# Optimization experiments

Measured on AMD Instinct MI355X. Metric: run time of the kernel, lower is better.

Reference implementation:

```python
import jax, jax.numpy as jnp
import numpy as np
from jax import lax

B, C, H, W = 2, 128, 192, 192
HEADS, WS, SS = 4, 8, 4
HID = 256  # int(C * expansion=2.0)
EPS = 1e-6


def _rpe_index(ws):
    coords = np.stack(np.meshgrid(np.arange(ws), np.arange(ws), indexing='ij')).reshape(2, -1)
    rel = (coords[:, :, None] - coords[:, None, :]).transpose(1, 2, 0)
    rel[:, :, 0] += ws - 1
    rel[:, :, 1] += ws - 1
    rel[:, :, 0] *= 2 * ws - 1
    return rel.sum(-1)  # (ws^2, ws^2) int index into rpe_table

RPE_IDX = _rpe_index(WS)


def _attn_mask(hp, wp, ws, ss):
    # Swin-style shifted-window mask, built once for static (hp, wp).
    img = np.zeros((hp, wp))
    cnt = 0
    for hs in (slice(0, -ws), slice(-ws, -ss), slice(-ss, None)):
        for wsl in (slice(0, -ws), slice(-ws, -ss), slice(-ss, None)):
            img[hs, wsl] = cnt
            cnt += 1
    mw = img.reshape(hp // ws, ws, wp // ws, ws).transpose(0, 2, 1, 3).reshape(-1, ws * ws)
    am = mw[:, None, :] - mw[:, :, None]
    return np.where(am != 0, -np.inf, 0.0).astype(np.float32)

MASK = jnp.asarray(_attn_mask(H, W, WS, SS))  # (nW, T, T)


def rmsnorm(x, s, b):
    # RMSNorm2d: variance over channel dim, computed in fp32.
    var = jnp.mean(jnp.square(x.astype(jnp.float32)), axis=1, keepdims=True)
    rms = jnp.sqrt(var + EPS).astype(x.dtype)
    return s[None, :, None, None] * x / rms + b[None, :, None, None]


def conv1x1(x, w, b):
    return jnp.einsum('oc,bchw->bohw', w, x) + b[None, :, None, None]


def dwconv3x3(x, w, b):
    y = lax.conv_general_dilated(x, w, (1, 1), 'SAME', feature_group_count=w.shape[0],
                                 dimension_numbers=('NCHW', 'OIHW', 'NCHW'))
    return y + b[None, :, None, None]


def gelu(x):
    return jax.nn.gelu(x, approximate=False)  # matches torch nn.GELU default (erf)


def conv_gated_block(x, s, b, w1, b1, wd, bd, w2, b2, beta):
    y = rmsnorm(x, s, b)
    y = conv1x1(y, w1, b1)
    y = dwconv3x3(y, wd, bd)
    u, v = jnp.split(y, 2, axis=1)
    y = conv1x1(u * gelu(v), w2, b2)
    return x + beta * y


def gated_ffn(x, s, b, w1, b1, w2, b2, gamma):
    y = rmsnorm(x, s, b)
    y = conv1x1(y, w1, b1)
    u, v = jnp.split(y, 2, axis=1)
    y = conv1x1(u * gelu(v), w2, b2)
    return x + gamma * y


def window_attention(x, qkv_w, qkv_b, rpe_table, proj_w, proj_b):
    b, c, h, w = x.shape
    hd = c // HEADS
    ws, ws2 = WS, WS * WS
    # H, W chosen divisible by ws, so _pad_to_window is a no-op here.
    x = jnp.roll(x, (-SS, -SS), axis=(2, 3))
    qkv = jnp.einsum('oc,bchw->bhwo', qkv_w, x) + qkv_b  # (B,H,W,3C)
    qkv = qkv.reshape(b, h // ws, ws, w // ws, ws, 3 * c).transpose(0, 1, 3, 2, 4, 5)
    qkv = qkv.reshape(-1, ws2, 3, HEADS, hd).transpose(2, 0, 3, 1, 4)  # (3, B*nW, nh, T, hd)
    q, k, v = qkv[0], qkv[1], qkv[2]
    attn = jnp.einsum('wnqd,wnkd->wnqk', q, k) * (hd ** -0.5)
    rpe = rpe_table[RPE_IDX.reshape(-1)].reshape(ws2, ws2, HEADS).transpose(2, 0, 1)  # (nh,T,T)
    nW = (h // ws) * (w // ws)
    attn = attn.reshape(b, nW, HEADS, ws2, ws2) + rpe[None, None] + MASK[None, :, None]
    attn = jax.nn.softmax(attn, axis=-1).reshape(-1, HEADS, ws2, ws2)
    out = jnp.einsum('wnqk,wnkd->wnqd', attn, v)
    out = out.transpose(0, 2, 1, 3).reshape(-1, ws2, c)
    out = out @ proj_w.T + proj_b  # nn.Linear
    out = out.reshape(b, h // ws, w // ws, ws, ws, c).transpose(0, 1, 3, 2, 4, 5).reshape(b, h, w, c)
    out = jnp.roll(out, (SS, SS), axis=(1, 2))
    return out.transpose(0, 3, 1, 2)


def setup_inputs():
    key = jax.random.key(0)
    ks = jax.random.split(key, 10)
    f = jnp.float32

    def nrm(k, shape, std=0.02):
        return jax.random.normal(k, shape, dtype=f) * std

    return {
        'x': jax.random.normal(ks[0], (B, C, H, W), dtype=f),
        'cg_s': jnp.ones((C,), f), 'cg_b': jnp.zeros((C,), f),
        'pw1_w': nrm(ks[1], (2 * HID, C)), 'pw1_b': jnp.zeros((2 * HID,), f),
        'dw_w': nrm(ks[2], (2 * HID, 1, 3, 3)), 'dw_b': jnp.zeros((2 * HID,), f),
        'pw2_w': nrm(ks[3], (C, HID)), 'pw2_b': jnp.zeros((C,), f),
        'beta': jnp.float32(0.5),
        'at_s': jnp.ones((C,), f), 'at_b': jnp.zeros((C,), f),
        'qkv_w': nrm(ks[4], (3 * C, C)), 'qkv_b': jnp.zeros((3 * C,), f),
        'rpe_table': nrm(ks[5], ((2 * WS - 1) ** 2, HEADS)),
        'proj_w': nrm(ks[6], (C, C)), 'proj_b': jnp.zeros((C,), f),
        'alpha': jnp.float32(0.5),
        'ff_s': jnp.ones((C,), f), 'ff_b': jnp.zeros((C,), f),
        'fc1_w': nrm(ks[7], (2 * HID, C)), 'fc1_b': jnp.zeros((2 * HID,), f),
        'fc2_w': nrm(ks[8], (C, HID)), 'fc2_b': jnp.zeros((C,), f),
        'gamma': jnp.float32(0.5),
    }


def reference(x, cg_s, cg_b, pw1_w, pw1_b, dw_w, dw_b, pw2_w, pw2_b, beta,
              at_s, at_b, qkv_w, qkv_b, rpe_table, proj_w, proj_b, alpha,
              ff_s, ff_b, fc1_w, fc1_b, fc2_w, fc2_b, gamma):
    x = conv_gated_block(x, cg_s, cg_b, pw1_w, pw1_b, dw_w, dw_b, pw2_w, pw2_b, beta)
    x = x + alpha * window_attention(rmsnorm(x, at_s, at_b), qkv_w, qkv_b, rpe_table, proj_w, proj_b)
    x = gated_ffn(x, ff_s, ff_b, fc1_w, fc1_b, fc2_w, fc2_b, gamma)
    return x
```

## Files before the change

### kernel.cpp

```cpp
#include <hip/hip_runtime.h>
#include <hip/hip_bf16.h>
#include <math.h>

#define HW   36864
#define BHW  73728

typedef float f32x4 __attribute__((ext_vector_type(4)));
typedef short short8 __attribute__((ext_vector_type(8)));
typedef short s16x4 __attribute__((ext_vector_type(4)));

__device__ __forceinline__ unsigned f2bf(float f) {
    unsigned u = __float_as_uint(f);
    return (u + 0x7fffu + ((u >> 16) & 1u)) >> 16;
}
__device__ __forceinline__ float bf2f(unsigned short s) {
    return __uint_as_float(((unsigned)s) << 16);
}
__device__ __forceinline__ float gelu_fast(float x) {
    float y = 1.5957691216057308f * fmaf(0.044715f * x * x, x, x);
    return x / (1.0f + __expf(-y));
}

__global__ __launch_bounds__(256)
void wconv_kernel(const float* __restrict__ w1, const float* __restrict__ w2,
                  const float* __restrict__ wq, const float* __restrict__ wp,
                  const float* __restrict__ wf1, const float* __restrict__ wf2,
                  const float* __restrict__ dww, const float* __restrict__ fb1,
                  ushort* __restrict__ o1, ushort* __restrict__ o2, ushort* __restrict__ oq,
                  ushort* __restrict__ op, ushort* __restrict__ of1, ushort* __restrict__ of2,
                  float* __restrict__ dwt, float* __restrict__ bg)
{
    int i = blockIdx.x * 256 + threadIdx.x;
    if      (i <  65536) o1 [i         ] = (ushort)f2bf(w1 [i         ]);
    else if (i <  98304) o2 [i -  65536] = (ushort)f2bf(w2 [i -  65536]);
    else if (i < 147456) oq [i -  98304] = (ushort)f2bf(wq [i -  98304]);
    else if (i < 163840) op [i - 147456] = (ushort)f2bf(wp [i - 147456]);
    else if (i < 229376) {
        int j = i - 163840;
        int col = j >> 7, k = j & 127;
        of1[j] = (ushort)f2bf(wf1[((size_t)((col & 1) * 256 + (col >> 1))) * 128 + k]);
    }
    else if (i < 262144) of2[i - 229376] = (ushort)f2bf(wf2[i - 229376]);
    else if (i < 266752) {
        int j = i - 262144;
        int tap = j >> 9, c = j & 511;
        dwt[j] = dww[c * 9 + tap];
    }
    else if (i < 267264) {
        int j = i - 266752;
        bg[j] = fb1[(j & 1) * 256 + (j >> 1)];
    }
}

__global__ __launch_bounds__(256)
void rmsnorm_t_kernel(const float* __restrict__ src, const float* __restrict__ s,
                      const float* __restrict__ bi, __hip_bfloat16* __restrict__ dst)
{
    __shared__ float sPar[4][64];
    __shared__ float sInv[64];
    int t = threadIdx.x, lane = t & 63, wv = t >> 6;
    int P = blockIdx.x * 64 + lane;
    int b = P / HW, pp = P - b * HW;
    const float* xb = src + (size_t)b * 128 * HW + pp;
    float v[32];
    float ss = 0.f;
#pragma unroll
    for (int i = 0; i < 32; ++i) {
        float x = xb[(size_t)(wv * 32 + i) * HW];
        v[i] = x;
        ss = fmaf(x, x, ss);
    }
    sPar[wv][lane] = ss;
    __syncthreads();
    if (t < 64) {
        float tot = sPar[0][t] + sPar[1][t] + sPar[2][t] + sPar[3][t];
        sInv[t] = 1.0f / sqrtf(tot * 0.0078125f + 1e-6f);
    }
    __syncthreads();
    float inv = sInv[lane];
    unsigned* drow = (unsigned*)(dst + (size_t)P * 128) + wv * 16;
#pragma unroll
    for (int i = 0; i < 32; i += 2) {
        int c = wv * 32 + i;
        float v0 = fmaf(s[c]     * v[i],     inv, bi[c]);
        float v1 = fmaf(s[c + 1] * v[i + 1], inv, bi[c + 1]);
        drow[i >> 1] = f2bf(v0) | (f2bf(v1) << 16);
    }
}

template<int K, int MODE>
__global__ __launch_bounds__(256, 3)
void gemm_kernel(const __hip_bfloat16* __restrict__ Abf, const __hip_bfloat16* __restrict__ Wbf,
                 const float* __restrict__ bias, int N,
                 __hip_bfloat16* __restrict__ outb)
{
    constexpr int STEPS = K / 32;
    __shared__ __align__(16) short smem[(64 + 128) * K];
    short* sA = smem;
    short* sB = smem + 64 * K;

    const short* A = (const short*)Abf;
    const short* W = (const short*)Wbf;

    int t = threadIdx.x;
    int lane = t & 63, wv = t >> 6;
    int m0 = blockIdx.x * 64;
    int n0 = blockIdx.y * 128;
    int q = lane >> 4, r16 = lane & 15;

    f32x4 acc[4][2];
#pragma unroll
    for (int nt = 0; nt < 2; ++nt) {
        float bv = bias[n0 + wv * 32 + nt * 16 + r16];
#pragma unroll
        for (int mt = 0; mt < 4; ++mt) acc[mt][nt] = (f32x4){bv, bv, bv, bv};
    }

    {
        int lr = lane >> 2, lk = lane & 3;
#pragma unroll
        for (int st = 0; st < STEPS; ++st) {
            int rowA = wv * 16 + lr;
            int kcA = lk ^ ((rowA >> 1) & 3);
            const short* ga = A + (size_t)(m0 + rowA) * K + st * 32 + kcA * 8;
            __builtin_amdgcn_global_load_lds((const __attribute__((address_space(1))) void*)ga,
                                             (__attribute__((address_space(3))) void*)(sA + st * 2048 + wv * 512), 16, 0, 0);
#pragma unroll
            for (int i = 0; i < 2; ++i) {
                int rb = wv * 32 + i * 16;
                int rowB = rb + lr;
                int kcB = lk ^ ((rowB >> 1) & 3);
                const short* gb = W + (size_t)(n0 + rowB) * K + st * 32 + kcB * 8;
                __builtin_amdgcn_global_load_lds((const __attribute__((address_space(1))) void*)gb,
                                                 (__attribute__((address_space(3))) void*)(sB + st * 4096 + rb * 32), 16, 0, 0);
            }
        }
    }
    __syncthreads();

#pragma unroll
    for (int st = 0; st < STEPS; ++st) {
        short8 af[4], bf[2];
#pragma unroll
        for (int mt = 0; mt < 4; ++mt) {
            int r = mt * 16 + r16;
            af[mt] = *(const short8*)(sA + st * 2048 + (r * 4 + (q ^ ((r >> 1) & 3))) * 8);
        }
#pragma unroll
        for (int nt = 0; nt < 2; ++nt) {
            int r = wv * 32 + nt * 16 + r16;
            bf[nt] = *(const short8*)(sB + st * 4096 + (r * 4 + (q ^ ((r >> 1) & 3))) * 8);
        }
#pragma unroll
        for (int mt = 0; mt < 4; ++mt)
#pragma unroll
            for (int nt = 0; nt < 2; ++nt)
                acc[mt][nt] = __builtin_amdgcn_mfma_f32_16x16x32_bf16(af[mt], bf[nt], acc[mt][nt], 0, 0, 0);
    }

    if constexpr (MODE == 0) {
        ushort* ob = (ushort*)outb;
#pragma unroll
        for (int mt = 0; mt < 4; ++mt) {
            int row0 = m0 + mt * 16 + q * 4;
#pragma unroll
            for (int nt = 0; nt < 2; ++nt) {
                int col = n0 + wv * 32 + nt * 16 + r16;
#pragma unroll
                for (int rg = 0; rg < 4; ++rg)
                    ob[(size_t)(row0 + rg) * N + col] = (ushort)f2bf(acc[mt][nt][rg]);
            }
        }
    } else {
        ushort* ob = (ushort*)outb;
        int parity = r16 & 1;
#pragma unroll
        for (int mt = 0; mt < 4; ++mt) {
            int row0 = m0 + mt * 16 + q * 4;
#pragma unroll
            for (int nt = 0; nt < 2; ++nt) {
                int ch = (n0 + wv * 32 + nt * 16 + r16) >> 1;
#pragma unroll
                for (int rg = 0; rg < 4; ++rg) {
                    float val = acc[mt][nt][rg];
                    float part = __shfl_xor(val, 1);
                    float uu = parity ? part : val;
                    float vv = parity ? val : part;
                    float g = uu * gelu_fast(vv);
                    if (!parity)
                        ob[(size_t)(row0 + rg) * 256 + ch] = (ushort)f2bf(g);
                }
            }
        }
    }
}

template<int K, bool RMS>
__global__ __launch_bounds__(256, 3)
void gemm_n128_kernel(const __hip_bfloat16* __restrict__ Abf, const __hip_bfloat16* __restrict__ Wbf,
                      const float* __restrict__ bias,
                      const float* __restrict__ rsrc, float* __restrict__ rdst,
                      const float* __restrict__ scale,
                      const float* __restrict__ rms_s, const float* __restrict__ rms_b,
                      __hip_bfloat16* __restrict__ xn)
{
    constexpr int NH = K / 128;
    __shared__ __align__(16) char smem[49152];
    short* sA = (short*)smem;
    short* sB = sA + 8192;
    float* sEp = (float*)smem;
    float* sPar = (float*)(smem + 34816);
    float* sInv = (float*)(smem + 39168);

    const short* A = (const short*)Abf;
    const short* W = (const short*)Wbf;

    int t = threadIdx.x;
    int lane = t & 63, wv = t >> 6;
    int m0 = blockIdx.x * 64;
    int q = lane >> 4, r16 = lane & 15;

    f32x4 acc[4][2];
#pragma unroll
    for (int nt = 0; nt < 2; ++nt) {
        float bv = bias[wv * 32 + nt * 16 + r16];
#pragma unroll
        for (int mt = 0; mt < 4; ++mt) acc[mt][nt] = (f32x4){bv, bv, bv, bv};
    }

#pragma unroll
    for (int h = 0; h < NH; ++h) {
        if (h) __syncthreads();
        {
            int lr = lane >> 2, lk = lane & 3;
#pragma unroll
            for (int st = 0; st < 4; ++st) {
                int kk = h * 128 + st * 32;
                int rowA = wv * 16 + lr;
                int kcA = lk ^ ((rowA >> 1) & 3);
                const short* ga = A + (size_t)(m0 + rowA) * K + kk + kcA * 8;
                __builtin_amdgcn_global_load_lds((const __attribute__((address_space(1))) void*)ga,
                                                 (__attribute__((address_space(3))) void*)(sA + st * 2048 + wv * 512), 16, 0, 0);
#pragma unroll
                for (int i = 0; i < 2; ++i) {
                    int rb = wv * 32 + i * 16;
                    int rowB = rb + lr;
                    int kcB = lk ^ ((rowB >> 1) & 3);
                    const short* gb = W + (size_t)rowB * K + kk + kcB * 8;
                    __builtin_amdgcn_global_load_lds((const __attribute__((address_space(1))) void*)gb,
                                                     (__attribute__((address_space(3))) void*)(sB + st * 4096 + rb * 32), 16, 0, 0);
                }
            }
        }
        __syncthreads();

#pragma unroll
        for (int st = 0; st < 4; ++st) {
            short8 af[4], bf[2];
#pragma unroll
            for (int mt = 0; mt < 4; ++mt) {
                int r = mt * 16 + r16;
                af[mt] = *(const short8*)(sA + st * 2048 + (r * 4 + (q ^ ((r >> 1) & 3))) * 8);
            }
#pragma unroll
            for (int nt = 0; nt < 2; ++nt) {
                int r = wv * 32 + nt * 16 + r16;
                bf[nt] = *(const short8*)(sB + st * 4096 + (r * 4 + (q ^ ((r >> 1) & 3))) * 8);
            }
#pragma unroll
            for (int mt = 0; mt < 4; ++mt)
#pragma unroll
                for (int nt = 0; nt < 2; ++nt)
                    acc[mt][nt] = __builtin_amdgcn_mfma_f32_16x16x32_bf16(af[mt], bf[nt], acc[mt][nt], 0, 0, 0);
        }
    }
    __syncthreads();

#pragma unroll
    for (int mt = 0; mt < 4; ++mt)
#pragma unroll
        for (int nt = 0; nt < 2; ++nt) {
            int c = wv * 32 + nt * 16 + r16;
            int px = mt * 16 + q * 4;
#pragma unroll
            for (int rg = 0; rg < 4; ++rg)
                sEp[c * 68 + px + rg] = acc[mt][nt][rg];
        }
    __syncthreads();

    int c16 = t >> 4, l16 = t & 15;
    int p0 = m0 + l16 * 4;
    int b = p0 / HW, pp = p0 - b * HW;
    float sc = scale[0];
    f32x4 ov[8];
    f32x4 ps = (f32x4){0.f, 0.f, 0.f, 0.f};
#pragma unroll
    for (int i = 0; i < 8; ++i) {
        int c = c16 + i * 16;
        f32x4 v = *(const f32x4*)&sEp[c * 68 + l16 * 4];
        size_t gi = (size_t)(b * 128 + c) * HW + pp;
        f32x4 r = *(const f32x4*)&rsrc[gi];
        f32x4 o = r + sc * v;
        *(f32x4*)&rdst[gi] = o;
        if constexpr (RMS) {
            ov[i] = o;
#pragma unroll
            for (int rg = 0; rg < 4; ++rg) ps[rg] = fmaf(o[rg], o[rg], ps[rg]);
        }
    }
    if constexpr (RMS) {
#pragma unroll
        for (int rg = 0; rg < 4; ++rg) sPar[(l16 * 4 + rg) * 17 + c16] = ps[rg];
        __syncthreads();
        if (t < 64) {
            float ssum = 0.f;
#pragma unroll
            for (int j = 0; j < 16; ++j) ssum += sPar[t * 17 + j];
            sInv[t] = 1.0f / sqrtf(ssum * 0.0078125f + 1e-6f);
        }
        __syncthreads();
        float iv[4];
#pragma unroll
        for (int rg = 0; rg < 4; ++rg) iv[rg] = sInv[l16 * 4 + rg];
        ushort* sXn = (ushort*)smem;
#pragma unroll
        for (int i = 0; i < 8; ++i) {
            int c = c16 + i * 16;
            float scs = rms_s[c], bcs = rms_b[c];
#pragma unroll
            for (int rg = 0; rg < 4; ++rg)
                sXn[(l16 * 4 + rg) * 132 + c] = (ushort)f2bf(fmaf(scs * ov[i][rg], iv[rg], bcs));
        }
        __syncthreads();
        {
            int px = t >> 2, qd = t & 3;
            const ushort* src = sXn + px * 132 + qd * 32;
            ushort* dst = (ushort*)xn + (size_t)(m0 + px) * 128 + qd * 32;
#pragma unroll
            for (int g = 0; g < 4; ++g)
                *(short8*)(dst + g * 8) = *(const short8*)(src + g * 8);
        }
    }
}

template<bool EDGE>
__device__ __forceinline__ void dw_body(const ushort* __restrict__ t1u,
                                        int b, int h0, int w, int cu,
                                        const f32x4* __restrict__ wu, const f32x4* __restrict__ wv,
                                        f32x4* __restrict__ au, f32x4* __restrict__ av)
{
#pragma unroll
    for (int r = 0; r < 6; ++r) {
        int hh = h0 - 1 + r;
        bool okr = EDGE ? ((unsigned)hh < 192u) : true;
        int hhc = (EDGE && !okr) ? 0 : hh;
#pragma unroll
        for (int dxi = 0; dxi < 3; ++dxi) {
            int w2 = w + dxi - 1;
            bool ok = EDGE ? (okr && ((unsigned)w2 < 192u)) : true;
            int w2c = EDGE ? ((w2 < 0) ? 0 : ((w2 > 191) ? 191 : w2)) : w2;
            const ushort* p = t1u + (size_t)(b * HW + hhc * 192 + w2c) * 512 + cu;
            s16x4 u4 = *(const s16x4*)p;
            s16x4 v4 = *(const s16x4*)(p + 256);
            f32x4 uf, vf;
#pragma unroll
            for (int e = 0; e < 4; ++e) {
                float uu = bf2f((ushort)u4[e]);
                float vv = bf2f((ushort)v4[e]);
                uf[e] = (EDGE && !ok) ? 0.f : uu;
                vf[e] = (EDGE && !ok) ? 0.f : vv;
            }
#pragma unroll
            for (int py = 0; py < 4; ++py) {
                int dy = r - 1 - py;
                if (dy < -1 || dy > 1) continue;
                int tap = (dy + 1) * 3 + dxi;
#pragma unroll
                for (int e = 0; e < 4; ++e) {
                    au[py][e] = fmaf(wu[tap][e], uf[e], au[py][e]);
                    av[py][e] = fmaf(wv[tap][e], vf[e], av[py][e]);
                }
            }
        }
    }
}

__global__ __launch_bounds__(256, 3)
void dwgate_kernel(const __hip_bfloat16* __restrict__ t1, const float* __restrict__ dwt,
                   const float* __restrict__ dwb, __hip_bfloat16* __restrict__ tg)
{
    int t = threadIdx.x;
    int tc = t & 63;
    int tp = t >> 6;
    int bx = blockIdx.x;
    int b = bx / 2304; int tt = bx % 2304;
    int th = tt / 48, tw = tt % 48;
    int h0 = th * 4, w = tw * 4 + tp;
    int cu = tc * 4;
    const ushort* t1u = (const ushort*)t1;

    f32x4 wu[9], wv[9];
#pragma unroll
    for (int tap = 0; tap < 9; ++tap) {
        wu[tap] = *(const f32x4*)(dwt + tap * 512 + cu);
        wv[tap] = *(const f32x4*)(dwt + tap * 512 + 256 + cu);
    }
    f32x4 bu = *(const f32x4*)(dwb + cu);
    f32x4 bv = *(const f32x4*)(dwb + 256 + cu);

    f32x4 au[4], av[4];
#pragma unroll
    for (int py = 0; py < 4; ++py) { au[py] = bu; av[py] = bv; }

    if (th > 0 && th < 47 && tw > 0 && tw < 47)
        dw_body<false>(t1u, b, h0, w, cu, wu, wv, au, av);
    else
        dw_body<true >(t1u, b, h0, w, cu, wu, wv, au, av);

#pragma unroll
    for (int py = 0; py < 4; ++py) {
        s16x4 o4;
#pragma unroll
        for (int e = 0; e < 4; ++e) o4[e] = (short)(ushort)f2bf(au[py][e] * gelu_fast(av[py][e]));
        int gp = b * HW + (h0 + py) * 192 + w;
        *(s16x4*)((ushort*)tg + (size_t)gp * 256 + cu) = o4;
    }
}

__device__ __forceinline__ int wpix(int wh, int ww, int m) {
    int ty = m >> 3, tx = m & 7;
    int hs = wh * 8 + ty + 4; if (hs >= 192) hs -= 192;
    int wsc = ww * 8 + tx + 4; if (wsc >= 192) wsc -= 192;
    return hs * 192 + wsc;
}
__device__ __forceinline__ int wreg(int wh, int ww, int m) {
    int hr = wh * 8 + (m >> 3), wr = ww * 8 + (m & 7);
    return ((hr < 184) ? 0 : (hr < 188) ? 1 : 2) * 3 +
           ((wr < 184) ? 0 : (wr < 188) ? 1 : 2);
}

__global__ __launch_bounds__(256)
void attn_kernel(const __hip_bfloat16* __restrict__ qkv, const float* __restrict__ rpe,
                 __hip_bfloat16* __restrict__ attnout)
{
    __shared__ char smem[54288];
    int t = threadIdx.x;
    int lane = t & 63, head = t >> 6;
    int wh = blockIdx.x / 24, ww = blockIdx.x % 24;
    int b = blockIdx.y;
    int q = lane >> 4, r16 = lane & 15;

    float* rpe_s = (float*)(smem + 50688);
    for (int i = t; i < 900; i += 256) rpe_s[i] = rpe[i];

    char* Pbuf  = smem + head * 12672;
    char* VTbuf = Pbuf + 8448;
    const ushort* qkvu = (const ushort*)qkv;

    short8 aq[4], bk[4];
#pragma unroll
    for (int mt = 0; mt < 4; ++mt) {
        int pix = wpix(wh, ww, mt * 16 + r16);
        const ushort* rowp = qkvu + (size_t)(b * HW + pix) * 384 + head * 32 + q * 8;
        aq[mt] = *(const short8*)rowp;
        bk[mt] = *(const short8*)(rowp + 128);
    }
    {
        int pix = wpix(wh, ww, lane);
        const ushort* vp = qkvu + (size_t)(b * HW + pix) * 384 + 256 + head * 32;
        ushort* vt = (ushort*)VTbuf;
#pragma unroll
        for (int g = 0; g < 4; ++g) {
            short8 v8 = *(const short8*)(vp + g * 8);
#pragma unroll
            for (int e = 0; e < 8; ++e) vt[(g * 8 + e) * 66 + lane] = (ushort)v8[e];
        }
    }
    __syncthreads();

    f32x4 s[4][4];
#pragma unroll
    for (int mt = 0; mt < 4; ++mt)
#pragma unroll
        for (int nt = 0; nt < 4; ++nt) s[mt][nt] = (f32x4){0.f, 0.f, 0.f, 0.f};
#pragma unroll
    for (int mt = 0; mt < 4; ++mt)
#pragma unroll
        for (int nt = 0; nt < 4; ++nt)
            s[mt][nt] = __builtin_amdgcn_mfma_f32_16x16x32_bf16(aq[mt], bk[nt], s[mt][nt], 0, 0, 0);

    bool edge = (wh == 23) || (ww == 23);
    int tyj[4], txj[4], rgj[4];
#pragma unroll
    for (int nt = 0; nt < 4; ++nt) {
        int j = nt * 16 + r16;
        tyj[nt] = j >> 3; txj[nt] = j & 7;
        rgj[nt] = wreg(wh, ww, j);
    }
    float rinv[4][4];
#pragma unroll
    for (int mt = 0; mt < 4; ++mt) {
#pragma unroll
        for (int rg = 0; rg < 4; ++rg) {
            int i = mt * 16 + q * 4 + rg;
            int tyi = i >> 3, txi = i & 7;
            int rgi = edge ? wreg(wh, ww, i) : 0;
            float mx = -INFINITY;
#pragma unroll
            for (int nt = 0; nt < 4; ++nt) {
                float v = s[mt][nt][rg] * 0.17677669529663689f
                        + rpe_s[((tyi - tyj[nt] + 7) * 15 + (txi - txj[nt] + 7)) * 4 + head];
                if (edge && rgi != rgj[nt]) v = -INFINITY;
                s[mt][nt][rg] = v;
                mx = fmaxf(mx, v);
            }
            mx = fmaxf(mx, __shfl_xor(mx, 1));
            mx = fmaxf(mx, __shfl_xor(mx, 2));
            mx = fmaxf(mx, __shfl_xor(mx, 4));
            mx = fmaxf(mx, __shfl_xor(mx, 8));
            float sum = 0.f;
#pragma unroll
            for (int nt = 0; nt < 4; ++nt) {
                float e = __expf(s[mt][nt][rg] - mx);
                s[mt][nt][rg] = e;
                sum += e;
            }
            sum += __shfl_xor(sum, 1);
            sum += __shfl_xor(sum, 2);
            sum += __shfl_xor(sum, 4);
            sum += __shfl_xor(sum, 8);
            rinv[mt][rg] = 1.0f / sum;
        }
    }

    ushort* Pu = (ushort*)Pbuf;
#pragma unroll
    for (int mt = 0; mt < 4; ++mt)
#pragma unroll
        for (int rg = 0; rg < 4; ++rg) {
            int i = mt * 16 + q * 4 + rg;
#pragma unroll
            for (int nt = 0; nt < 4; ++nt)
                Pu[i * 66 + nt * 16 + r16] = (ushort)f2bf(s[mt][nt][rg]);
        }
    __syncthreads();

    f32x4 o[4][2];
#pragma unroll
    for (int mt = 0; mt < 4; ++mt) { o[mt][0] = (f32x4){0,0,0,0}; o[mt][1] = (f32x4){0,0,0,0}; }
    const uint* Pw = (const uint*)Pbuf;
    const uint* Vw = (const uint*)VTbuf;
#pragma unroll
    for (int ks = 0; ks < 2; ++ks) {
        short8 ap[4];
#pragma unroll
        for (int mt = 0; mt < 4; ++mt) {
            int base = (mt * 16 + r16) * 33 + ks * 16 + q * 4;
            uint d0 = Pw[base], d1 = Pw[base + 1], d2 = Pw[base + 2], d3 = Pw[base + 3];
            union { uint u[4]; short8 s8; } cv; cv.u[0] = d0; cv.u[1] = d1; cv.u[2] = d2; cv.u[3] = d3;
            ap[mt] = cv.s8;
        }
        short8 bv[2];
#pragma unroll
        for (int nt = 0; nt < 2; ++nt) {
            int base = (nt * 16 + r16) * 33 + ks * 16 + q * 4;
            uint d0 = Vw[base], d1 = Vw[base + 1], d2 = Vw[base + 2], d3 = Vw[base + 3];
            union { uint u[4]; short8 s8; } cv; cv.u[0] = d0; cv.u[1] = d1; cv.u[2] = d2; cv.u[3] = d3;
            bv[nt] = cv.s8;
        }
#pragma unroll
        for (int mt = 0; mt < 4; ++mt)
#pragma unroll
            for (int nt = 0; nt < 2; ++nt)
                o[mt][nt] = __builtin_amdgcn_mfma_f32_16x16x32_bf16(ap[mt], bv[nt], o[mt][nt], 0, 0, 0);
    }
    __syncthreads();

    float* Of = (float*)Pbuf;
#pragma unroll
    for (int mt = 0; mt < 4; ++mt)
#pragma unroll
        for (int rg = 0; rg < 4; ++rg) {
            int i = mt * 16 + q * 4 + rg;
            float sc = rinv[mt][rg];
            Of[i * 33 + r16]      = o[mt][0][rg] * sc;
            Of[i * 33 + 16 + r16] = o[mt][1][rg] * sc;
        }
    __syncthreads();
    {
        int pix = wpix(wh, ww, lane);
        ushort* ob = (ushort*)attnout + (size_t)(b * HW + pix) * 128 + head * 32;
#pragma unroll
        for (int g = 0; g < 4; ++g) {
            short8 o8;
#pragma unroll
            for (int e = 0; e < 8; ++e) o8[e] = (short)(ushort)f2bf(Of[lane * 33 + g * 8 + e]);
            *(short8*)(ob + g * 8) = o8;
        }
    }
}

extern "C" void kernel_launch(void* const* d_in, const int* in_sizes, int n_in,
                              void* d_out, int out_size, void* d_ws, size_t ws_size,
                              hipStream_t stream)
{
    const float* x     = (const float*)d_in[0];
    const float* cg_s  = (const float*)d_in[1];
    const float* cg_b  = (const float*)d_in[2];
    const float* pw1_w = (const float*)d_in[3];
    const float* pw1_b = (const float*)d_in[4];
    const float* dw_w  = (const float*)d_in[5];
    const float* dw_b  = (const float*)d_in[6];
    const float* pw2_w = (const float*)d_in[7];
    const float* pw2_b = (const float*)d_in[8];
    const float* beta  = (const float*)d_in[9];
    const float* at_s  = (const float*)d_in[10];
    const float* at_b  = (const float*)d_in[11];
    const float* qkv_w = (const float*)d_in[12];
    const float* qkv_b = (const float*)d_in[13];
    const float* rpe   = (const float*)d_in[14];
    const float* proj_w= (const float*)d_in[15];
    const float* proj_b= (const float*)d_in[16];
    const float* alpha = (const float*)d_in[17];
    const float* ff_s  = (const float*)d_in[18];
    const float* ff_b  = (const float*)d_in[19];
    const float* fc1_w = (const float*)d_in[20];
    const float* fc1_b = (const float*)d_in[21];
    const float* fc2_w = (const float*)d_in[22];
    const float* fc2_b = (const float*)d_in[23];
    const float* gamma = (const float*)d_in[24];
    float* out = (float*)d_out;

    char* ws = (char*)d_ws;
    __hip_bfloat16* Xn    = (__hip_bfloat16*)ws;
    __hip_bfloat16* t1    = (__hip_bfloat16*)(ws + 18874368);
    __hip_bfloat16* qkvb  = t1;
    __hip_bfloat16* tg    = (__hip_bfloat16*)(ws + 94371840);
    __hip_bfloat16* attno = tg;
    char* wsw = ws + 132120576;
    ushort* w1b  = (ushort*)(wsw);
    ushort* w2b  = (ushort*)(wsw + 131072);
    ushort* wqb  = (ushort*)(wsw + 196608);
    ushort* wpb  = (ushort*)(wsw + 294912);
    ushort* wf1b = (ushort*)(wsw + 327680);
    ushort* wf2b = (ushort*)(wsw + 458752);
    float*  dwt  = (float*) (wsw + 524288);
    float*  bg1  = (float*) (wsw + 542720);

    wconv_kernel<<<1044, 256, 0, stream>>>(pw1_w, pw2_w, qkv_w, proj_w, fc1_w, fc2_w, dw_w, fc1_b,
                                           w1b, w2b, wqb, wpb, wf1b, wf2b, dwt, bg1);

    rmsnorm_t_kernel<<<1152, 256, 0, stream>>>(x, cg_s, cg_b, Xn);
    gemm_kernel<128, 0><<<dim3(1152, 4), 256, 0, stream>>>(Xn, (__hip_bfloat16*)w1b, pw1_b, 512, t1);
    dwgate_kernel<<<4608, 256, 0, stream>>>(t1, dwt, dw_b, tg);
    gemm_n128_kernel<256, true><<<1152, 256, 0, stream>>>(tg, (__hip_bfloat16*)w2b, pw2_b,
                                                          x, out, beta, at_s, at_b, Xn);

    gemm_kernel<128, 0><<<dim3(1152, 3), 256, 0, stream>>>(Xn, (__hip_bfloat16*)wqb, qkv_b, 384, qkvb);
    attn_kernel<<<dim3(576, 2), 256, 0, stream>>>(qkvb, rpe, attno);
    gemm_n128_kernel<128, true><<<1152, 256, 0, stream>>>(attno, (__hip_bfloat16*)wpb, proj_b,
                                                          out, out, alpha, ff_s, ff_b, Xn);

    gemm_kernel<128, 2><<<dim3(1152, 4), 256, 0, stream>>>(Xn, (__hip_bfloat16*)wf1b, bg1, 512, tg);
    gemm_n128_kernel<256, false><<<1152, 256, 0, stream>>>(tg, (__hip_bfloat16*)wf2b, fc2_b,
                                                           out, out, gamma, nullptr, nullptr, nullptr);
}
```

Before: 360.1 us.

## Load GEMM weight fragments into registers and remap depthwise-gate threads

Result: slower. 446.5 us (+24.0%).

```diff
diff --git a/kernel.cpp b/kernel.cpp
--- a/kernel.cpp
+++ b/kernel.cpp
@@ -6,6 +6,7 @@
 #define BHW  73728
 
 typedef float f32x4 __attribute__((ext_vector_type(4)));
+typedef float f32x2 __attribute__((ext_vector_type(2)));
 typedef short short8 __attribute__((ext_vector_type(8)));
 typedef short s16x4 __attribute__((ext_vector_type(4)));
 
@@ -89,15 +90,13 @@
 }
 
 template<int K, int MODE>
-__global__ __launch_bounds__(256, 3)
+__global__ __launch_bounds__(256, 4)
 void gemm_kernel(const __hip_bfloat16* __restrict__ Abf, const __hip_bfloat16* __restrict__ Wbf,
                  const float* __restrict__ bias, int N,
                  __hip_bfloat16* __restrict__ outb)
 {
     constexpr int STEPS = K / 32;
-    __shared__ __align__(16) short smem[(64 + 128) * K];
-    short* sA = smem;
-    short* sB = smem + 64 * K;
+    __shared__ __align__(16) short sA[64 * K];
 
     const short* A = (const short*)Abf;
     const short* W = (const short*)Wbf;
@@ -108,54 +107,47 @@
     int n0 = blockIdx.y * 128;
     int q = lane >> 4, r16 = lane & 15;
 
-    f32x4 acc[4][2];
-#pragma unroll
-    for (int nt = 0; nt < 2; ++nt) {
-        float bv = bias[n0 + wv * 32 + nt * 16 + r16];
-#pragma unroll
-        for (int mt = 0; mt < 4; ++mt) acc[mt][nt] = (f32x4){bv, bv, bv, bv};
-    }
-
     {
         int lr = lane >> 2, lk = lane & 3;
+        int rowA = wv * 16 + lr;
+        int kcA = lk ^ ((rowA >> 1) & 3);
 #pragma unroll
         for (int st = 0; st < STEPS; ++st) {
-            int rowA = wv * 16 + lr;
-            int kcA = lk ^ ((rowA >> 1) & 3);
             const short* ga = A + (size_t)(m0 + rowA) * K + st * 32 + kcA * 8;
             __builtin_amdgcn_global_load_lds((const __attribute__((address_space(1))) void*)ga,
                                              (__attribute__((address_space(3))) void*)(sA + st * 2048 + wv * 512), 16, 0, 0);
-#pragma unroll
-            for (int i = 0; i < 2; ++i) {
-                int rb = wv * 32 + i * 16;
-                int rowB = rb + lr;
-                int kcB = lk ^ ((rowB >> 1) & 3);
-                const short* gb = W + (size_t)(n0 + rowB) * K + st * 32 + kcB * 8;
-                __builtin_amdgcn_global_load_lds((const __attribute__((address_space(1))) void*)gb,
-                                                 (__attribute__((address_space(3))) void*)(sB + st * 4096 + rb * 32), 16, 0, 0);
-            }
-        }
+        }
+    }
+
+    short8 bfr[STEPS][2];
+#pragma unroll
+    for (int st = 0; st < STEPS; ++st)
+#pragma unroll
+        for (int nt = 0; nt < 2; ++nt)
+            bfr[st][nt] = *(const short8*)(W + (size_t)(n0 + wv * 32 + nt * 16 + r16) * K + st * 32 + q * 8);
+
+    f32x4 acc[4][2];
+#pragma unroll
+    for (int nt = 0; nt < 2; ++nt) {
+        float bv = bias[n0 + wv * 32 + nt * 16 + r16];
+#pragma unroll
+        for (int mt = 0; mt < 4; ++mt) acc[mt][nt] = (f32x4){bv, bv, bv, bv};
     }
     __syncthreads();
 
 #pragma unroll
     for (int st = 0; st < STEPS; ++st) {
-        short8 af[4], bf[2];
+        short8 af[4];
 #pragma unroll
         for (int mt = 0; mt < 4; ++mt) {
             int r = mt * 16 + r16;
             af[mt] = *(const short8*)(sA + st * 2048 + (r * 4 + (q ^ ((r >> 1) & 3))) * 8);
         }
 #pragma unroll
-        for (int nt = 0; nt < 2; ++nt) {
-            int r = wv * 32 + nt * 16 + r16;
-            bf[nt] = *(const short8*)(sB + st * 4096 + (r * 4 + (q ^ ((r >> 1) & 3))) * 8);
-        }
-#pragma unroll
         for (int mt = 0; mt < 4; ++mt)
 #pragma unroll
             for (int nt = 0; nt < 2; ++nt)
-                acc[mt][nt] = __builtin_amdgcn_mfma_f32_16x16x32_bf16(af[mt], bf[nt], acc[mt][nt], 0, 0, 0);
+                acc[mt][nt] = __builtin_amdgcn_mfma_f32_16x16x32_bf16(af[mt], bfr[st][nt], acc[mt][nt], 0, 0, 0);
     }
 
     if constexpr (MODE == 0) {
@@ -196,7 +188,7 @@
 }
 
 template<int K, bool RMS>
-__global__ __launch_bounds__(256, 3)
+__global__ __launch_bounds__(256, 4)
 void gemm_n128_kernel(const __hip_bfloat16* __restrict__ Abf, const __hip_bfloat16* __restrict__ Wbf,
                       const float* __restrict__ bias,
                       const float* __restrict__ rsrc, float* __restrict__ rdst,
@@ -205,9 +197,9 @@
                       __hip_bfloat16* __restrict__ xn)
 {
     constexpr int NH = K / 128;
-    __shared__ __align__(16) char smem[49152];
+    constexpr int SMEM = RMS ? 39424 : 34816;
+    __shared__ __align__(16) char smem[SMEM];
     short* sA = (short*)smem;
-    short* sB = sA + 8192;
     float* sEp = (float*)smem;
     float* sPar = (float*)(smem + 34816);
     float* sInv = (float*)(smem + 39168);
@@ -219,6 +211,9 @@
     int lane = t & 63, wv = t >> 6;
     int m0 = blockIdx.x * 64;
     int q = lane >> 4, r16 = lane & 15;
+    int lr = lane >> 2, lk = lane & 3;
+    int rowA = wv * 16 + lr;
+    int kcA = lk ^ ((rowA >> 1) & 3);
 
     f32x4 acc[4][2];
 #pragma unroll
@@ -231,47 +226,33 @@
 #pragma unroll
     for (int h = 0; h < NH; ++h) {
         if (h) __syncthreads();
-        {
-            int lr = lane >> 2, lk = lane & 3;
-#pragma unroll
-            for (int st = 0; st < 4; ++st) {
-                int kk = h * 128 + st * 32;
-                int rowA = wv * 16 + lr;
-                int kcA = lk ^ ((rowA >> 1) & 3);
-                const short* ga = A + (size_t)(m0 + rowA) * K + kk + kcA * 8;
-                __builtin_amdgcn_global_load_lds((const __attribute__((address_space(1))) void*)ga,
-                                                 (__attribute__((address_space(3))) void*)(sA + st * 2048 + wv * 512), 16, 0, 0);
-#pragma unroll
-                for (int i = 0; i < 2; ++i) {
-                    int rb = wv * 32 + i * 16;
-                    int rowB = rb + lr;
-                    int kcB = lk ^ ((rowB >> 1) & 3);
-                    const short* gb = W + (size_t)rowB * K + kk + kcB * 8;
-                    __builtin_amdgcn_global_load_lds((const __attribute__((address_space(1))) void*)gb,
-                                                     (__attribute__((address_space(3))) void*)(sB + st * 4096 + rb * 32), 16, 0, 0);
-                }
-            }
-        }
+#pragma unroll
+        for (int st = 0; st < 4; ++st) {
+            const short* ga = A + (size_t)(m0 + rowA) * K + h * 128 + st * 32 + kcA * 8;
+            __builtin_amdgcn_global_load_lds((const __attribute__((address_space(1))) void*)ga,
+                                             (__attribute__((address_space(3))) void*)(sA + st * 2048 + wv * 512), 16, 0, 0);
+        }
+        short8 bfr[4][2];
+#pragma unroll
+        for (int st = 0; st < 4; ++st)
+#pragma unroll
+            for (int nt = 0; nt < 2; ++nt)
+                bfr[st][nt] = *(const short8*)(W + (size_t)(wv * 32 + nt * 16 + r16) * K + h * 128 + st * 32 + q * 8);
         __syncthreads();
 
 #pragma unroll
         for (int st = 0; st < 4; ++st) {
-            short8 af[4], bf[2];
+            short8 af[4];
 #pragma unroll
             for (int mt = 0; mt < 4; ++mt) {
                 int r = mt * 16 + r16;
                 af[mt] = *(const short8*)(sA + st * 2048 + (r * 4 + (q ^ ((r >> 1) & 3))) * 8);
             }
 #pragma unroll
-            for (int nt = 0; nt < 2; ++nt) {
-                int r = wv * 32 + nt * 16 + r16;
-                bf[nt] = *(const short8*)(sB + st * 4096 + (r * 4 + (q ^ ((r >> 1) & 3))) * 8);
-            }
-#pragma unroll
             for (int mt = 0; mt < 4; ++mt)
 #pragma unroll
                 for (int nt = 0; nt < 2; ++nt)
-                    acc[mt][nt] = __builtin_amdgcn_mfma_f32_16x16x32_bf16(af[mt], bf[nt], acc[mt][nt], 0, 0, 0);
+                    acc[mt][nt] = __builtin_amdgcn_mfma_f32_16x16x32_bf16(af[mt], bfr[st][nt], acc[mt][nt], 0, 0, 0);
         }
     }
     __syncthreads();
@@ -344,10 +325,10 @@
 }
 
 template<bool EDGE>
-__device__ __forceinline__ void dw_body(const ushort* __restrict__ t1u,
-                                        int b, int h0, int w, int cu,
-                                        const f32x4* __restrict__ wu, const f32x4* __restrict__ wv,
-                                        f32x4* __restrict__ au, f32x4* __restrict__ av)
+__device__ __forceinline__ void dw_body2(const ushort* __restrict__ t1u,
+                                         int b, int h0, int w, int cu,
+                                         const f32x2* __restrict__ wu, const f32x2* __restrict__ wv,
+                                         f32x2* __restrict__ au, f32x2* __restrict__ av)
 {
 #pragma unroll
     for (int r = 0; r < 6; ++r) {
@@ -360,23 +341,19 @@
             bool ok = EDGE ? (okr && ((unsigned)w2 < 192u)) : true;
             int w2c = EDGE ? ((w2 < 0) ? 0 : ((w2 > 191) ? 191 : w2)) : w2;
             const ushort* p = t1u + (size_t)(b * HW + hhc * 192 + w2c) * 512 + cu;
-            s16x4 u4 = *(const s16x4*)p;
-            s16x4 v4 = *(const s16x4*)(p + 256);
-            f32x4 uf, vf;
-#pragma unroll
-            for (int e = 0; e < 4; ++e) {
-                float uu = bf2f((ushort)u4[e]);
-                float vv = bf2f((ushort)v4[e]);
-                uf[e] = (EDGE && !ok) ? 0.f : uu;
-                vf[e] = (EDGE && !ok) ? 0.f : vv;
-            }
+            uint u2 = *(const uint*)p;
+            uint v2 = *(const uint*)(p + 256);
+            f32x2 uf, vf;
+            uf[0] = bf2f((ushort)(u2 & 0xffffu)); uf[1] = bf2f((ushort)(u2 >> 16));
+            vf[0] = bf2f((ushort)(v2 & 0xffffu)); vf[1] = bf2f((ushort)(v2 >> 16));
+            if (EDGE && !ok) { uf = (f32x2){0.f, 0.f}; vf = (f32x2){0.f, 0.f}; }
 #pragma unroll
             for (int py = 0; py < 4; ++py) {
                 int dy = r - 1 - py;
                 if (dy < -1 || dy > 1) continue;
                 int tap = (dy + 1) * 3 + dxi;
 #pragma unroll
-                for (int e = 0; e < 4; ++e) {
+                for (int e = 0; e < 2; ++e) {
                     au[py][e] = fmaf(wu[tap][e], uf[e], au[py][e]);
                     av[py][e] = fmaf(wv[tap][e], vf[e], av[py][e]);
                 }
@@ -385,45 +362,45 @@
     }
 }
 
-__global__ __launch_bounds__(256, 3)
+__global__ __launch_bounds__(256, 5)
 void dwgate_kernel(const __hip_bfloat16* __restrict__ t1, const float* __restrict__ dwt,
                    const float* __restrict__ dwb, __hip_bfloat16* __restrict__ tg)
 {
     int t = threadIdx.x;
-    int tc = t & 63;
-    int tp = t >> 6;
-    int bx = blockIdx.x;
-    int b = bx / 2304; int tt = bx % 2304;
-    int th = tt / 48, tw = tt % 48;
-    int h0 = th * 4, w = tw * 4 + tp;
-    int cu = tc * 4;
+    int tc = t & 127;
+    int tp = t >> 7;
+    int bx0 = blockIdx.x;
+    int bx = (bx0 & 7) * 1152 + (bx0 >> 3);
+    int b = bx / 4608; int tt = bx - b * 4608;
+    int th = tt / 96, tw = tt - th * 96;
+    int h0 = th * 4, w = tw * 2 + tp;
+    int cu = tc * 2;
     const ushort* t1u = (const ushort*)t1;
 
-    f32x4 wu[9], wv[9];
+    f32x2 wu[9], wv[9];
 #pragma unroll
     for (int tap = 0; tap < 9; ++tap) {
-        wu[tap] = *(const f32x4*)(dwt + tap * 512 + cu);
-        wv[tap] = *(const f32x4*)(dwt + tap * 512 + 256 + cu);
-    }
-    f32x4 bu = *(const f32x4*)(dwb + cu);
-    f32x4 bv = *(const f32x4*)(dwb + 256 + cu);
-
-    f32x4 au[4], av[4];
+        wu[tap] = *(const f32x2*)(dwt + tap * 512 + cu);
+        wv[tap] = *(const f32x2*)(dwt + tap * 512 + 256 + cu);
+    }
+    f32x2 bu = *(const f32x2*)(dwb + cu);
+    f32x2 bv = *(const f32x2*)(dwb + 256 + cu);
+
+    f32x2 au[4], av[4];
 #pragma unroll
     for (int py = 0; py < 4; ++py) { au[py] = bu; av[py] = bv; }
 
-    if (th > 0 && th < 47 && tw > 0 && tw < 47)
-        dw_body<false>(t1u, b, h0, w, cu, wu, wv, au, av);
+    if (th > 0 && th < 47 && tw > 0 && tw < 95)
+        dw_body2<false>(t1u, b, h0, w, cu, wu, wv, au, av);
     else
-        dw_body<true >(t1u, b, h0, w, cu, wu, wv, au, av);
+        dw_body2<true >(t1u, b, h0, w, cu, wu, wv, au, av);
 
 #pragma unroll
     for (int py = 0; py < 4; ++py) {
-        s16x4 o4;
-#pragma unroll
-        for (int e = 0; e < 4; ++e) o4[e] = (short)(ushort)f2bf(au[py][e] * gelu_fast(av[py][e]));
+        uint o = f2bf(au[py][0] * gelu_fast(av[py][0]))
+               | (f2bf(au[py][1] * gelu_fast(av[py][1])) << 16);
         int gp = b * HW + (h0 + py) * 192 + w;
-        *(s16x4*)((ushort*)tg + (size_t)gp * 256 + cu) = o4;
+        *(uint*)((ushort*)tg + (size_t)gp * 256 + cu) = o;
     }
 }
 
@@ -652,7 +629,7 @@
 
     rmsnorm_t_kernel<<<1152, 256, 0, stream>>>(x, cg_s, cg_b, Xn);
     gemm_kernel<128, 0><<<dim3(1152, 4), 256, 0, stream>>>(Xn, (__hip_bfloat16*)w1b, pw1_b, 512, t1);
-    dwgate_kernel<<<4608, 256, 0, stream>>>(t1, dwt, dw_b, tg);
+    dwgate_kernel<<<9216, 256, 0, stream>>>(t1, dwt, dw_b, tg);
     gemm_n128_kernel<256, true><<<1152, 256, 0, stream>>>(tg, (__hip_bfloat16*)w2b, pw2_b,
                                                           x, out, beta, at_s, at_b, Xn);
 
```
